# Kernel optimization log

Hardware: AMD Instinct MI355X
Metric: run time of the kernel (lower is better)

## Reference

```python
import jax, jax.numpy as jnp
import numpy as np

N_NODES = 50000
N_EDGES = 600000
D_IN = 128
DIM = 128
N_REL = 3
N_LAYERS = 2


def setup_inputs() -> dict:
    key = jax.random.key(0)
    ks = jax.random.split(key, 10)
    s = 1.0 / np.sqrt(DIM)
    x = jax.random.normal(ks[0], (N_NODES, D_IN), dtype=jnp.float32)
    edge_index = jax.random.randint(ks[1], (2, N_EDGES), 0, N_NODES)
    edge_type = jax.random.randint(ks[2], (N_EDGES,), 0, N_REL)
    edge_weight = jax.random.uniform(ks[3], (N_EDGES,), dtype=jnp.float32)
    # stacked per-layer parameters (layer dims are uniform since D_IN == DIM)
    w_rel = jax.random.normal(ks[4], (N_LAYERS, N_REL, DIM, DIM), dtype=jnp.float32) * s
    w_root = jax.random.normal(ks[5], (N_LAYERS, DIM, DIM), dtype=jnp.float32) * s
    b_conv = jnp.zeros((N_LAYERS, DIM), dtype=jnp.float32)
    w_skip = jax.random.normal(ks[6], (N_LAYERS, D_IN, DIM), dtype=jnp.float32) * s
    b_skip = jnp.zeros((N_LAYERS, DIM), dtype=jnp.float32)
    return {"x": x, "edge_index": edge_index, "edge_type": edge_type,
            "edge_weight": edge_weight, "w_rel": w_rel, "w_root": w_root,
            "b_conv": b_conv, "w_skip": w_skip, "b_skip": b_skip}


def reference(x, edge_index, edge_type, edge_weight, w_rel, w_root, b_conv, w_skip, b_skip):
    n = x.shape[0]
    src, dst = edge_index[0], edge_index[1]
    h = x
    for l in range(w_rel.shape[0]):  # small fixed layer loop (2)
        skip = x @ w_skip[l] + b_skip[l]                      # [N, dim]
        # per-relation transform of all nodes: [R, N, dim] (cheap GEMMs),
        # avoids materializing a per-edge [E, d, d] weight gather
        hr = jnp.einsum('nd,rde->rne', h, w_rel[l])
        msgs = hr[edge_type, src] * edge_weight[:, None]      # [E, dim] gather
        agg = jax.ops.segment_sum(msgs, dst, num_segments=n)  # scatter-add
        h = agg + h @ w_root[l] + b_conv[l] + skip            # conv + skip residual
    return h
```

## Files before the change

### kernel.cpp

```cpp
#include <hip/hip_runtime.h>


#define DIM 128
#define MAXDEG 40
#define K_CNTB 512
#define K_CONVB 2048

typedef short short8 __attribute__((ext_vector_type(8)));
typedef float f32x4 __attribute__((ext_vector_type(4)));

__device__ __forceinline__ unsigned short f2bf(float f) {
    unsigned u = __float_as_uint(f);
    unsigned r = (u + 0x7FFFu + ((u >> 16) & 1u)) >> 16;
    return (unsigned short)r;
}
__device__ __forceinline__ float bflo(unsigned p) { return __uint_as_float(p << 16); }
__device__ __forceinline__ float bfhi(unsigned p) { return __uint_as_float(p & 0xFFFF0000u); }

__device__ void prep_body(const float* __restrict__ w_rel, const float* __restrict__ w_root,
                          const float* __restrict__ w_skip, unsigned short* __restrict__ WTf,
                          int bid) {
    for (int i = bid * 256 + threadIdx.x; i < 2 * 5 * DIM * DIM; i += 256 * 256) {
        int j    = i & 7;
        int lane = (i >> 3) & 63;
        int ks   = (i >> 9) & 3;
        int n    = (i >> 11) & 7;
        int s    = (i >> 14) % 5;
        int l    = i / (5 * DIM * DIM);
        int col = n * 16 + (lane & 15);
        int k   = ks * 32 + (lane >> 4) * 8 + j;
        float v;
        if (s < 3)       v = w_rel[(((size_t)l * 3 + s) * DIM + k) * DIM + col];
        else if (s == 3) {
            v = w_root[((size_t)l * DIM + k) * DIM + col];
            if (l == 0) v += w_skip[((size_t)k) * DIM + col];
        } else           v = w_skip[((size_t)l * DIM + k) * DIM + col];
        WTf[i] = f2bf(v);
    }
}

__global__ __launch_bounds__(256) void prep_zero(
    const float* __restrict__ w_rel, const float* __restrict__ w_root,
    const float* __restrict__ w_skip, unsigned short* __restrict__ WTf,
    int4* __restrict__ zp, int n4) {
    int b = blockIdx.x;
    if (b < 256) prep_body(w_rel, w_root, w_skip, WTf, b);
    else {
        int i = (b - 256) * 256 + threadIdx.x;
        if (i < n4) zp[i] = make_int4(0, 0, 0, 0);
    }
}

__device__ void conv_body(const float* __restrict__ in, unsigned short* __restrict__ ob,
                          int n8, int bid) {
    for (int i = bid * 256 + threadIdx.x; i < n8; i += K_CONVB * 256) {
        const float4* ip = reinterpret_cast<const float4*>(in) + (size_t)i * 2;
        float4 v0 = ip[0], v1 = ip[1];
        uint4 o;
        o.x = (unsigned)f2bf(v0.x) | ((unsigned)f2bf(v0.y) << 16);
        o.y = (unsigned)f2bf(v0.z) | ((unsigned)f2bf(v0.w) << 16);
        o.z = (unsigned)f2bf(v1.x) | ((unsigned)f2bf(v1.y) << 16);
        o.w = (unsigned)f2bf(v1.z) | ((unsigned)f2bf(v1.w) << 16);
        reinterpret_cast<uint4*>(ob)[i] = o;
    }
}

__device__ void cntsct_body(const int* __restrict__ src, const int* __restrict__ dst,
                            const int* __restrict__ etype, const float* __restrict__ ew,
                            int* __restrict__ counts, unsigned* __restrict__ csrp,
                            int E, int bid) {
    for (int i = bid * 256 + threadIdx.x; i < E; i += K_CNTB * 256) {
        int d = dst[i];
        int r = atomicAdd(&counts[d], 1);
        unsigned wq = (unsigned)__float2uint_rn(ew[i] * 16383.0f);
        unsigned rec = (unsigned)src[i] | ((unsigned)etype[i] << 16) | (wq << 18);
        if (r < MAXDEG) csrp[(size_t)d * MAXDEG + r] = rec;
    }
}

template<bool HAS_SKIP, bool AF32>
__device__ void gemm_body(
    int bid,
    const void* __restrict__ Ap, const unsigned short* __restrict__ Xb,
    const unsigned short* __restrict__ WTf,
    const float* __restrict__ bconv, const float* __restrict__ bskip,
    unsigned short* __restrict__ hr, void* __restrict__ outp, int M) {
    constexpr int NF = HAS_SKIP ? 40 : 32;
    __shared__ unsigned short stile[4][32][136];
    int t = threadIdx.x, lane = t & 63, wid = t >> 6;
    int lrow = lane & 15, lhi = lane >> 4;
    int r0 = bid * 128 + wid * 32;

    short8 af[2][4];
    #pragma unroll
    for (int rg = 0; rg < 2; ++rg) {
        int r = r0 + rg * 16 + lrow;
        int rc = r < M ? r : 0;
        if (AF32) {
            const float* ap = (const float*)Ap + (size_t)rc * DIM + lhi * 8;
            #pragma unroll
            for (int ks = 0; ks < 4; ++ks) {
                float4 u = *reinterpret_cast<const float4*>(ap + ks * 32);
                float4 v = *reinterpret_cast<const float4*>(ap + ks * 32 + 4);
                short8 s;
                s[0] = (short)f2bf(u.x); s[1] = (short)f2bf(u.y);
                s[2] = (short)f2bf(u.z); s[3] = (short)f2bf(u.w);
                s[4] = (short)f2bf(v.x); s[5] = (short)f2bf(v.y);
                s[6] = (short)f2bf(v.z); s[7] = (short)f2bf(v.w);
                af[rg][ks] = s;
            }
        } else {
            const unsigned short* ap = (const unsigned short*)Ap + (size_t)rc * DIM + lhi * 8;
            #pragma unroll
            for (int ks = 0; ks < 4; ++ks)
                af[rg][ks] = *reinterpret_cast<const short8*>(ap + ks * 32);
        }
    }
    short8 xf[2][4];
    f32x4 acc34[2][8];

    auto flush = [&](unsigned short* gbase) {
        #pragma unroll
        for (int j = 0; j < 8; ++j) {
            int lr = j * 4 + lhi;
            int lc = lrow * 8;
            int gr = r0 + lr;
            if (gr < M)
                *reinterpret_cast<uint4*>(gbase + (size_t)gr * DIM + lc) =
                    *reinterpret_cast<const uint4*>(&stile[wid][lr][lc]);
        }
    };

    short8 b0[4], b1[4];
    auto loadB = [&](int fi, short8* bb) {
        const unsigned short* p = WTf + ((size_t)fi * 4 * 64 + lane) * 8;
        #pragma unroll
        for (int ks = 0; ks < 4; ++ks)
            bb[ks] = *reinterpret_cast<const short8*>(p + ks * 512);
    };
    loadB(0, b0);
    #pragma unroll
    for (int fi = 0; fi < NF; ++fi) {
        short8* bc = (fi & 1) ? b1 : b0;
        short8* bn = (fi & 1) ? b0 : b1;
        if (fi + 1 < NF) loadB(fi + 1, bn);
        const int slot = fi >> 3, n = fi & 7;
        const int col = n * 16 + lrow;
        if (HAS_SKIP && slot == 3 && n == 0) {
            #pragma unroll
            for (int rg = 0; rg < 2; ++rg) {
                int r = r0 + rg * 16 + lrow;
                const unsigned short* xp = Xb + (size_t)(r < M ? r : 0) * DIM + lhi * 8;
                #pragma unroll
                for (int ks = 0; ks < 4; ++ks)
                    xf[rg][ks] = *reinterpret_cast<const short8*>(xp + ks * 32);
            }
        }
        if (slot < 3) {
            f32x4 a0 = {0.f, 0.f, 0.f, 0.f}, a1 = {0.f, 0.f, 0.f, 0.f};
            #pragma unroll
            for (int ks = 0; ks < 4; ++ks) {
                a0 = __builtin_amdgcn_mfma_f32_16x16x32_bf16(af[0][ks], bc[ks], a0, 0, 0, 0);
                a1 = __builtin_amdgcn_mfma_f32_16x16x32_bf16(af[1][ks], bc[ks], a1, 0, 0, 0);
            }
            #pragma unroll
            for (int rg = 0; rg < 2; ++rg) {
                f32x4& aa = rg ? a1 : a0;
                #pragma unroll
                for (int i2 = 0; i2 < 4; ++i2)
                    stile[wid][rg * 16 + lhi * 4 + i2][col] = f2bf(aa[i2]);
            }
            if (n == 7) flush(hr + (size_t)slot * M * DIM);
        } else if (!HAS_SKIP) {
            f32x4 a0 = {0.f, 0.f, 0.f, 0.f}, a1 = {0.f, 0.f, 0.f, 0.f};
            #pragma unroll
            for (int ks = 0; ks < 4; ++ks) {
                a0 = __builtin_amdgcn_mfma_f32_16x16x32_bf16(af[0][ks], bc[ks], a0, 0, 0, 0);
                a1 = __builtin_amdgcn_mfma_f32_16x16x32_bf16(af[1][ks], bc[ks], a1, 0, 0, 0);
            }
            float bb = bconv[col] + bskip[col];
            #pragma unroll
            for (int rg = 0; rg < 2; ++rg) {
                f32x4& aa = rg ? a1 : a0;
                #pragma unroll
                for (int i2 = 0; i2 < 4; ++i2)
                    stile[wid][rg * 16 + lhi * 4 + i2][col] = f2bf(aa[i2] + bb);
            }
            if (n == 7) flush((unsigned short*)outp);
        } else if (slot == 3) {
            f32x4 z = {0.f, 0.f, 0.f, 0.f};
            acc34[0][n] = z; acc34[1][n] = z;
            #pragma unroll
            for (int ks = 0; ks < 4; ++ks) {
                acc34[0][n] = __builtin_amdgcn_mfma_f32_16x16x32_bf16(af[0][ks], bc[ks], acc34[0][n], 0, 0, 0);
                acc34[1][n] = __builtin_amdgcn_mfma_f32_16x16x32_bf16(af[1][ks], bc[ks], acc34[1][n], 0, 0, 0);
            }
        } else {
            #pragma unroll
            for (int ks = 0; ks < 4; ++ks) {
                acc34[0][n] = __builtin_amdgcn_mfma_f32_16x16x32_bf16(xf[0][ks], bc[ks], acc34[0][n], 0, 0, 0);
                acc34[1][n] = __builtin_amdgcn_mfma_f32_16x16x32_bf16(xf[1][ks], bc[ks], acc34[1][n], 0, 0, 0);
            }
            float bb = bconv[col] + bskip[col];
            float* op = (float*)outp;
            #pragma unroll
            for (int rg = 0; rg < 2; ++rg) {
                #pragma unroll
                for (int i2 = 0; i2 < 4; ++i2) {
                    int r = r0 + rg * 16 + lhi * 4 + i2;
                    if (r < M) op[(size_t)r * DIM + col] = acc34[rg][n][i2] + bb;
                }
            }
        }
    }
}

__global__ __launch_bounds__(256) void fat1_kernel(
    const float* __restrict__ x, const unsigned short* __restrict__ WTf,
    const float* __restrict__ bconv, const float* __restrict__ bskip,
    unsigned short* __restrict__ hr, unsigned short* __restrict__ h1, int M, int GB,
    const int* __restrict__ src, const int* __restrict__ dst,
    const int* __restrict__ etype, const float* __restrict__ ew,
    int* __restrict__ counts, unsigned* __restrict__ csrp, int E,
    unsigned short* __restrict__ xb, int n8) {
    int b = blockIdx.x;
    if (b < GB)
        gemm_body<false, true>(b, x, nullptr, WTf, bconv, bskip, hr, h1, M);
    else if (b < GB + K_CNTB)
        cntsct_body(src, dst, etype, ew, counts, csrp, E, b - GB);
    else
        conv_body(x, xb, n8, b - GB - K_CNTB);
}

__global__ __launch_bounds__(256) void gemm1_kernel(
    const unsigned short* __restrict__ Ab, const unsigned short* __restrict__ Xb,
    const unsigned short* __restrict__ WTf,
    const float* __restrict__ bconv, const float* __restrict__ bskip,
    unsigned short* __restrict__ hr, float* __restrict__ outp, int M) {
    gemm_body<true, false>(blockIdx.x, Ab, Xb, WTf, bconv, bskip, hr, outp, M);
}

template<bool BF16IO>
__global__ __launch_bounds__(256) void agg_kernel(
    const unsigned short* __restrict__ hr, const unsigned* __restrict__ csrp,
    const int* __restrict__ counts, float* __restrict__ outf,
    unsigned short* __restrict__ outb, int N) {
    int t = threadIdx.x;
    int lane = t & 63;
    int v = blockIdx.x * 4 + (t >> 6);
    if (v >= N) return;
    int g = lane >> 4;
    int l16 = lane & 15;
    int beg = v * MAXDEG;
    int cnt = counts[v]; if (cnt > MAXDEG) cnt = MAXDEG;
    int end = beg + cnt;

    float acc[8] = {0.f, 0.f, 0.f, 0.f, 0.f, 0.f, 0.f, 0.f};
    int iA = beg + g, iB = iA + 4;
    bool vA = iA < end, vB = iB < end;
    unsigned sA = vA ? csrp[iA] : 0u;
    unsigned sB = vB ? csrp[iB] : 0u;
    while (__any(vA)) {
        uint4 pA = make_uint4(0, 0, 0, 0), pB = make_uint4(0, 0, 0, 0);
        if (vA) {
            const unsigned short* row = hr + ((size_t)((sA >> 16) & 3) * N + (sA & 0xFFFF)) * DIM + l16 * 8;
            pA = *reinterpret_cast<const uint4*>(row);
        }
        if (vB) {
            const unsigned short* row = hr + ((size_t)((sB >> 16) & 3) * N + (sB & 0xFFFF)) * DIM + l16 * 8;
            pB = *reinterpret_cast<const uint4*>(row);
        }
        int nA = iA + 8, nB = iB + 8;
        bool nvA = nA < end, nvB = nB < end;
        unsigned nsA = nvA ? csrp[nA] : 0u;
        unsigned nsB = nvB ? csrp[nB] : 0u;
        if (vA) {
            float w = (float)(sA >> 18) * (1.0f / 16383.0f);
            acc[0] += w * bflo(pA.x); acc[1] += w * bfhi(pA.x);
            acc[2] += w * bflo(pA.y); acc[3] += w * bfhi(pA.y);
            acc[4] += w * bflo(pA.z); acc[5] += w * bfhi(pA.z);
            acc[6] += w * bflo(pA.w); acc[7] += w * bfhi(pA.w);
        }
        if (vB) {
            float w = (float)(sB >> 18) * (1.0f / 16383.0f);
            acc[0] += w * bflo(pB.x); acc[1] += w * bfhi(pB.x);
            acc[2] += w * bflo(pB.y); acc[3] += w * bfhi(pB.y);
            acc[4] += w * bflo(pB.z); acc[5] += w * bfhi(pB.z);
            acc[6] += w * bflo(pB.w); acc[7] += w * bfhi(pB.w);
        }
        iA = nA; iB = nB; sA = nsA; sB = nsB; vA = nvA; vB = nvB;
    }
    #pragma unroll
    for (int j = 0; j < 8; ++j) {
        acc[j] += __shfl_xor(acc[j], 16);
        acc[j] += __shfl_xor(acc[j], 32);
    }
    if (g == 0) {
        if (BF16IO) {
            unsigned short* op = outb + (size_t)v * DIM + l16 * 8;
            uint4 cur = *reinterpret_cast<const uint4*>(op);
            float r0 = bflo(cur.x) + acc[0], r1 = bfhi(cur.x) + acc[1];
            float r2 = bflo(cur.y) + acc[2], r3 = bfhi(cur.y) + acc[3];
            float r4 = bflo(cur.z) + acc[4], r5 = bfhi(cur.z) + acc[5];
            float r6 = bflo(cur.w) + acc[6], r7 = bfhi(cur.w) + acc[7];
            uint4 o;
            o.x = (unsigned)f2bf(r0) | ((unsigned)f2bf(r1) << 16);
            o.y = (unsigned)f2bf(r2) | ((unsigned)f2bf(r3) << 16);
            o.z = (unsigned)f2bf(r4) | ((unsigned)f2bf(r5) << 16);
            o.w = (unsigned)f2bf(r6) | ((unsigned)f2bf(r7) << 16);
            *reinterpret_cast<uint4*>(op) = o;
        } else {
            float* op = outf + (size_t)v * DIM + l16 * 8;
            float4 c0 = *reinterpret_cast<float4*>(op);
            float4 c1 = *reinterpret_cast<float4*>(op + 4);
            c0.x += acc[0]; c0.y += acc[1]; c0.z += acc[2]; c0.w += acc[3];
            c1.x += acc[4]; c1.y += acc[5]; c1.z += acc[6]; c1.w += acc[7];
            *reinterpret_cast<float4*>(op) = c0;
            *reinterpret_cast<float4*>(op + 4) = c1;
        }
    }
}

extern "C" void kernel_launch(void* const* d_in, const int* in_sizes, int n_in,
                              void* d_out, int out_size, void* d_ws, size_t ws_size,
                              hipStream_t stream) {
    const float* x       = (const float*)d_in[0];
    const int*   eidx    = (const int*)d_in[1];
    const int*   etype   = (const int*)d_in[2];
    const float* ew      = (const float*)d_in[3];
    const float* w_rel   = (const float*)d_in[4];
    const float* w_root  = (const float*)d_in[5];
    const float* b_conv  = (const float*)d_in[6];
    const float* w_skip  = (const float*)d_in[7];
    const float* b_skip  = (const float*)d_in[8];

    const int N = in_sizes[0] / DIM;
    const int E = in_sizes[3];
    const int* src = eidx;
    const int* dst = eidx + E;

    char* w = (char*)d_ws;
    unsigned short* WTf  = (unsigned short*)w;  w += (size_t)2 * 5 * DIM * DIM * 2;
    unsigned short* xb   = (unsigned short*)w;  w += (size_t)N * DIM * 2;
    unsigned short* hr   = (unsigned short*)w;  w += (size_t)3 * N * DIM * 2;
    unsigned short* h1   = (unsigned short*)w;  w += (size_t)N * DIM * 2;
    int* counts          = (int*)w;             w += (size_t)N * 4;
    unsigned* csrp       = (unsigned*)w;        w += (size_t)N * MAXDEG * 4;

    float* out = (float*)d_out;
    const int n8 = N * DIM / 8;
    const int zc = (N + 3) / 4;
    const int zblk = (zc + 255) / 256;

    prep_zero<<<256 + zblk, 256, 0, stream>>>(w_rel, w_root, w_skip, WTf,
                                              (int4*)counts, zc);
    int GB = (N + 127) / 128;
    fat1_kernel<<<GB + K_CNTB + K_CONVB, 256, 0, stream>>>(
        x, WTf, b_conv, b_skip, hr, h1, N, GB,
        src, dst, etype, ew, counts, csrp, E, xb, n8);
    int ablocks = (N + 3) / 4;
    agg_kernel<true><<<ablocks, 256, 0, stream>>>(hr, csrp, counts, nullptr, h1, N);
    gemm1_kernel<<<GB, 256, 0, stream>>>(h1, xb, WTf + (size_t)5 * DIM * DIM,
                                         b_conv + DIM, b_skip + DIM, hr, out, N);
    agg_kernel<false><<<ablocks, 256, 0, stream>>>(hr, csrp, counts, out, nullptr, N);
}
```

Measured before the change: 139.0 us.

## Overlap layer-1 skip GEMM with layer-0 aggregation in a fused launch

Pulls the layer-1 skip GEMM (x @ w_skip + biases) out of gemm1 and runs it in a new fat2 kernel alongside the layer-0 aggregation, since it depends only on x. gemm1 then computes only the relation and root transforms and adds the root result into the output in place. This shortens the critical-path GEMM and fills idle compute during the memory-bound aggregation. The cost is an extra read-modify-write of the fp32 output in gemm1.

```diff
diff --git a/kernel.cpp b/kernel.cpp
--- a/kernel.cpp
+++ b/kernel.cpp
@@ -78,14 +78,11 @@
     }
 }
 
-template<bool HAS_SKIP, bool AF32>
-__device__ void gemm_body(
-    int bid,
-    const void* __restrict__ Ap, const unsigned short* __restrict__ Xb,
+__device__ void gemm0_body(
+    int bid, const float* __restrict__ Ap,
     const unsigned short* __restrict__ WTf,
     const float* __restrict__ bconv, const float* __restrict__ bskip,
-    unsigned short* __restrict__ hr, void* __restrict__ outp, int M) {
-    constexpr int NF = HAS_SKIP ? 40 : 32;
+    unsigned short* __restrict__ hr, unsigned short* __restrict__ h1, int M) {
     __shared__ unsigned short stile[4][32][136];
     int t = threadIdx.x, lane = t & 63, wid = t >> 6;
     int lrow = lane & 15, lhi = lane >> 4;
@@ -96,41 +93,28 @@
     for (int rg = 0; rg < 2; ++rg) {
         int r = r0 + rg * 16 + lrow;
         int rc = r < M ? r : 0;
-        if (AF32) {
-            const float* ap = (const float*)Ap + (size_t)rc * DIM + lhi * 8;
-            #pragma unroll
-            for (int ks = 0; ks < 4; ++ks) {
-                float4 u = *reinterpret_cast<const float4*>(ap + ks * 32);
-                float4 v = *reinterpret_cast<const float4*>(ap + ks * 32 + 4);
-                short8 s;
-                s[0] = (short)f2bf(u.x); s[1] = (short)f2bf(u.y);
-                s[2] = (short)f2bf(u.z); s[3] = (short)f2bf(u.w);
-                s[4] = (short)f2bf(v.x); s[5] = (short)f2bf(v.y);
-                s[6] = (short)f2bf(v.z); s[7] = (short)f2bf(v.w);
-                af[rg][ks] = s;
-            }
-        } else {
-            const unsigned short* ap = (const unsigned short*)Ap + (size_t)rc * DIM + lhi * 8;
-            #pragma unroll
-            for (int ks = 0; ks < 4; ++ks)
-                af[rg][ks] = *reinterpret_cast<const short8*>(ap + ks * 32);
-        }
-    }
-    short8 xf[2][4];
-    f32x4 acc34[2][8];
-
+        const float* ap = Ap + (size_t)rc * DIM + lhi * 8;
+        #pragma unroll
+        for (int ks = 0; ks < 4; ++ks) {
+            float4 u = *reinterpret_cast<const float4*>(ap + ks * 32);
+            float4 v = *reinterpret_cast<const float4*>(ap + ks * 32 + 4);
+            short8 s;
+            s[0] = (short)f2bf(u.x); s[1] = (short)f2bf(u.y);
+            s[2] = (short)f2bf(u.z); s[3] = (short)f2bf(u.w);
+            s[4] = (short)f2bf(v.x); s[5] = (short)f2bf(v.y);
+            s[6] = (short)f2bf(v.z); s[7] = (short)f2bf(v.w);
+            af[rg][ks] = s;
+        }
+    }
     auto flush = [&](unsigned short* gbase) {
         #pragma unroll
         for (int j = 0; j < 8; ++j) {
-            int lr = j * 4 + lhi;
-            int lc = lrow * 8;
-            int gr = r0 + lr;
+            int lr = j * 4 + lhi, gr = r0 + lr;
             if (gr < M)
-                *reinterpret_cast<uint4*>(gbase + (size_t)gr * DIM + lc) =
-                    *reinterpret_cast<const uint4*>(&stile[wid][lr][lc]);
+                *reinterpret_cast<uint4*>(gbase + (size_t)gr * DIM + lrow * 8) =
+                    *reinterpret_cast<const uint4*>(&stile[wid][lr][lrow * 8]);
         }
     };
-
     short8 b0[4], b1[4];
     auto loadB = [&](int fi, short8* bb) {
         const unsigned short* p = WTf + ((size_t)fi * 4 * 64 + lane) * 8;
@@ -140,29 +124,19 @@
     };
     loadB(0, b0);
     #pragma unroll
-    for (int fi = 0; fi < NF; ++fi) {
+    for (int fi = 0; fi < 32; ++fi) {
         short8* bc = (fi & 1) ? b1 : b0;
         short8* bn = (fi & 1) ? b0 : b1;
-        if (fi + 1 < NF) loadB(fi + 1, bn);
+        if (fi + 1 < 32) loadB(fi + 1, bn);
         const int slot = fi >> 3, n = fi & 7;
         const int col = n * 16 + lrow;
-        if (HAS_SKIP && slot == 3 && n == 0) {
-            #pragma unroll
-            for (int rg = 0; rg < 2; ++rg) {
-                int r = r0 + rg * 16 + lrow;
-                const unsigned short* xp = Xb + (size_t)(r < M ? r : 0) * DIM + lhi * 8;
-                #pragma unroll
-                for (int ks = 0; ks < 4; ++ks)
-                    xf[rg][ks] = *reinterpret_cast<const short8*>(xp + ks * 32);
-            }
+        f32x4 a0 = {0.f, 0.f, 0.f, 0.f}, a1 = {0.f, 0.f, 0.f, 0.f};
+        #pragma unroll
+        for (int ks = 0; ks < 4; ++ks) {
+            a0 = __builtin_amdgcn_mfma_f32_16x16x32_bf16(af[0][ks], bc[ks], a0, 0, 0, 0);
+            a1 = __builtin_amdgcn_mfma_f32_16x16x32_bf16(af[1][ks], bc[ks], a1, 0, 0, 0);
         }
         if (slot < 3) {
-            f32x4 a0 = {0.f, 0.f, 0.f, 0.f}, a1 = {0.f, 0.f, 0.f, 0.f};
-            #pragma unroll
-            for (int ks = 0; ks < 4; ++ks) {
-                a0 = __builtin_amdgcn_mfma_f32_16x16x32_bf16(af[0][ks], bc[ks], a0, 0, 0, 0);
-                a1 = __builtin_amdgcn_mfma_f32_16x16x32_bf16(af[1][ks], bc[ks], a1, 0, 0, 0);
-            }
             #pragma unroll
             for (int rg = 0; rg < 2; ++rg) {
                 f32x4& aa = rg ? a1 : a0;
@@ -171,13 +145,7 @@
                     stile[wid][rg * 16 + lhi * 4 + i2][col] = f2bf(aa[i2]);
             }
             if (n == 7) flush(hr + (size_t)slot * M * DIM);
-        } else if (!HAS_SKIP) {
-            f32x4 a0 = {0.f, 0.f, 0.f, 0.f}, a1 = {0.f, 0.f, 0.f, 0.f};
-            #pragma unroll
-            for (int ks = 0; ks < 4; ++ks) {
-                a0 = __builtin_amdgcn_mfma_f32_16x16x32_bf16(af[0][ks], bc[ks], a0, 0, 0, 0);
-                a1 = __builtin_amdgcn_mfma_f32_16x16x32_bf16(af[1][ks], bc[ks], a1, 0, 0, 0);
-            }
+        } else {
             float bb = bconv[col] + bskip[col];
             #pragma unroll
             for (int rg = 0; rg < 2; ++rg) {
@@ -186,31 +154,7 @@
                 for (int i2 = 0; i2 < 4; ++i2)
                     stile[wid][rg * 16 + lhi * 4 + i2][col] = f2bf(aa[i2] + bb);
             }
-            if (n == 7) flush((unsigned short*)outp);
-        } else if (slot == 3) {
-            f32x4 z = {0.f, 0.f, 0.f, 0.f};
-            acc34[0][n] = z; acc34[1][n] = z;
-            #pragma unroll
-            for (int ks = 0; ks < 4; ++ks) {
-                acc34[0][n] = __builtin_amdgcn_mfma_f32_16x16x32_bf16(af[0][ks], bc[ks], acc34[0][n], 0, 0, 0);
-                acc34[1][n] = __builtin_amdgcn_mfma_f32_16x16x32_bf16(af[1][ks], bc[ks], acc34[1][n], 0, 0, 0);
-            }
-        } else {
-            #pragma unroll
-            for (int ks = 0; ks < 4; ++ks) {
-                acc34[0][n] = __builtin_amdgcn_mfma_f32_16x16x32_bf16(xf[0][ks], bc[ks], acc34[0][n], 0, 0, 0);
-                acc34[1][n] = __builtin_amdgcn_mfma_f32_16x16x32_bf16(xf[1][ks], bc[ks], acc34[1][n], 0, 0, 0);
-            }
-            float bb = bconv[col] + bskip[col];
-            float* op = (float*)outp;
-            #pragma unroll
-            for (int rg = 0; rg < 2; ++rg) {
-                #pragma unroll
-                for (int i2 = 0; i2 < 4; ++i2) {
-                    int r = r0 + rg * 16 + lhi * 4 + i2;
-                    if (r < M) op[(size_t)r * DIM + col] = acc34[rg][n][i2] + bb;
-                }
-            }
+            if (n == 7) flush(h1);
         }
     }
 }
@@ -225,29 +169,21 @@
     unsigned short* __restrict__ xb, int n8) {
     int b = blockIdx.x;
     if (b < GB)
-        gemm_body<false, true>(b, x, nullptr, WTf, bconv, bskip, hr, h1, M);
+        gemm0_body(b, x, WTf, bconv, bskip, hr, h1, M);
     else if (b < GB + K_CNTB)
         cntsct_body(src, dst, etype, ew, counts, csrp, E, b - GB);
     else
         conv_body(x, xb, n8, b - GB - K_CNTB);
 }
 
-__global__ __launch_bounds__(256) void gemm1_kernel(
-    const unsigned short* __restrict__ Ab, const unsigned short* __restrict__ Xb,
-    const unsigned short* __restrict__ WTf,
-    const float* __restrict__ bconv, const float* __restrict__ bskip,
-    unsigned short* __restrict__ hr, float* __restrict__ outp, int M) {
-    gemm_body<true, false>(blockIdx.x, Ab, Xb, WTf, bconv, bskip, hr, outp, M);
-}
-
 template<bool BF16IO>
-__global__ __launch_bounds__(256) void agg_kernel(
-    const unsigned short* __restrict__ hr, const unsigned* __restrict__ csrp,
+__device__ void agg_body(
+    int bid, const unsigned short* __restrict__ hr, const unsigned* __restrict__ csrp,
     const int* __restrict__ counts, float* __restrict__ outf,
     unsigned short* __restrict__ outb, int N) {
     int t = threadIdx.x;
     int lane = t & 63;
-    int v = blockIdx.x * 4 + (t >> 6);
+    int v = bid * 4 + (t >> 6);
     if (v >= N) return;
     int g = lane >> 4;
     int l16 = lane & 15;
@@ -321,6 +257,155 @@
     }
 }
 
+__device__ void skip1_body(int bid, const unsigned short* __restrict__ xb,
+                           const unsigned short* __restrict__ WTf1,
+                           const float* __restrict__ bconv, const float* __restrict__ bskip,
+                           float* __restrict__ out, int M) {
+    int t = threadIdx.x, lane = t & 63, wid = t >> 6;
+    int lrow = lane & 15, lhi = lane >> 4;
+    int r0 = bid * 128 + wid * 32;
+
+    short8 af[2][4];
+    #pragma unroll
+    for (int rg = 0; rg < 2; ++rg) {
+        int r = r0 + rg * 16 + lrow;
+        const unsigned short* ap = xb + (size_t)(r < M ? r : 0) * DIM + lhi * 8;
+        #pragma unroll
+        for (int ks = 0; ks < 4; ++ks)
+            af[rg][ks] = *reinterpret_cast<const short8*>(ap + ks * 32);
+    }
+    short8 b0[4], b1[4];
+    auto loadB = [&](int fi, short8* bb) {
+        const unsigned short* p = WTf1 + ((size_t)fi * 4 * 64 + lane) * 8;
+        #pragma unroll
+        for (int ks = 0; ks < 4; ++ks)
+            bb[ks] = *reinterpret_cast<const short8*>(p + ks * 512);
+    };
+    loadB(32, b0);
+    #pragma unroll
+    for (int n = 0; n < 8; ++n) {
+        short8* bc = (n & 1) ? b1 : b0;
+        short8* bn = (n & 1) ? b0 : b1;
+        if (n + 1 < 8) loadB(32 + n + 1, bn);
+        f32x4 a0 = {0.f, 0.f, 0.f, 0.f}, a1 = {0.f, 0.f, 0.f, 0.f};
+        #pragma unroll
+        for (int ks = 0; ks < 4; ++ks) {
+            a0 = __builtin_amdgcn_mfma_f32_16x16x32_bf16(af[0][ks], bc[ks], a0, 0, 0, 0);
+            a1 = __builtin_amdgcn_mfma_f32_16x16x32_bf16(af[1][ks], bc[ks], a1, 0, 0, 0);
+        }
+        int col = n * 16 + lrow;
+        float bb = bconv[col] + bskip[col];
+        #pragma unroll
+        for (int rg = 0; rg < 2; ++rg) {
+            f32x4& aa = rg ? a1 : a0;
+            #pragma unroll
+            for (int i2 = 0; i2 < 4; ++i2) {
+                int r = r0 + rg * 16 + lhi * 4 + i2;
+                if (r < M) out[(size_t)r * DIM + col] = aa[i2] + bb;
+            }
+        }
+    }
+}
+
+__global__ __launch_bounds__(256) void fat2_kernel(
+    const unsigned short* __restrict__ hr, const unsigned* __restrict__ csrp,
+    const int* __restrict__ counts, unsigned short* __restrict__ h1, int N, int AB,
+    const unsigned short* __restrict__ xb, const unsigned short* __restrict__ WTf1,
+    const float* __restrict__ bconv1, const float* __restrict__ bskip1,
+    float* __restrict__ out, int M) {
+    int b = blockIdx.x;
+    if (b < AB) agg_body<true>(b, hr, csrp, counts, nullptr, h1, N);
+    else        skip1_body(b - AB, xb, WTf1, bconv1, bskip1, out, M);
+}
+
+__global__ __launch_bounds__(256) void gemm1_kernel(
+    const unsigned short* __restrict__ Ab, const unsigned short* __restrict__ WTf1,
+    unsigned short* __restrict__ hr, float* __restrict__ outp, int M) {
+    __shared__ unsigned short stile[4][32][136];
+    int bid = blockIdx.x;
+    int t = threadIdx.x, lane = t & 63, wid = t >> 6;
+    int lrow = lane & 15, lhi = lane >> 4;
+    int r0 = bid * 128 + wid * 32;
+
+    short8 af[2][4];
+    #pragma unroll
+    for (int rg = 0; rg < 2; ++rg) {
+        int r = r0 + rg * 16 + lrow;
+        const unsigned short* ap = Ab + (size_t)(r < M ? r : 0) * DIM + lhi * 8;
+        #pragma unroll
+        for (int ks = 0; ks < 4; ++ks)
+            af[rg][ks] = *reinterpret_cast<const short8*>(ap + ks * 32);
+    }
+    f32x4 acc34[2][8];
+    auto flush = [&](unsigned short* gbase) {
+        #pragma unroll
+        for (int j = 0; j < 8; ++j) {
+            int lr = j * 4 + lhi, gr = r0 + lr;
+            if (gr < M)
+                *reinterpret_cast<uint4*>(gbase + (size_t)gr * DIM + lrow * 8) =
+                    *reinterpret_cast<const uint4*>(&stile[wid][lr][lrow * 8]);
+        }
+    };
+    short8 b0[4], b1[4];
+    auto loadB = [&](int fi, short8* bb) {
+        const unsigned short* p = WTf1 + ((size_t)fi * 4 * 64 + lane) * 8;
+        #pragma unroll
+        for (int ks = 0; ks < 4; ++ks)
+            bb[ks] = *reinterpret_cast<const short8*>(p + ks * 512);
+    };
+    loadB(0, b0);
+    #pragma unroll
+    for (int fi = 0; fi < 32; ++fi) {
+        short8* bc = (fi & 1) ? b1 : b0;
+        short8* bn = (fi & 1) ? b0 : b1;
+        if (fi + 1 < 32) loadB(fi + 1, bn);
+        const int slot = fi >> 3, n = fi & 7;
+        const int col = n * 16 + lrow;
+        if (slot < 3) {
+            f32x4 a0 = {0.f, 0.f, 0.f, 0.f}, a1 = {0.f, 0.f, 0.f, 0.f};
+            #pragma unroll
+            for (int ks = 0; ks < 4; ++ks) {
+                a0 = __builtin_amdgcn_mfma_f32_16x16x32_bf16(af[0][ks], bc[ks], a0, 0, 0, 0);
+                a1 = __builtin_amdgcn_mfma_f32_16x16x32_bf16(af[1][ks], bc[ks], a1, 0, 0, 0);
+            }
+            #pragma unroll
+            for (int rg = 0; rg < 2; ++rg) {
+                f32x4& aa = rg ? a1 : a0;
+                #pragma unroll
+                for (int i2 = 0; i2 < 4; ++i2)
+                    stile[wid][rg * 16 + lhi * 4 + i2][col] = f2bf(aa[i2]);
+            }
+            if (n == 7) flush(hr + (size_t)slot * M * DIM);
+        } else {
+            f32x4 z = {0.f, 0.f, 0.f, 0.f};
+            acc34[0][n] = z; acc34[1][n] = z;
+            #pragma unroll
+            for (int ks = 0; ks < 4; ++ks) {
+                acc34[0][n] = __builtin_amdgcn_mfma_f32_16x16x32_bf16(af[0][ks], bc[ks], acc34[0][n], 0, 0, 0);
+                acc34[1][n] = __builtin_amdgcn_mfma_f32_16x16x32_bf16(af[1][ks], bc[ks], acc34[1][n], 0, 0, 0);
+            }
+        }
+    }
+    #pragma unroll
+    for (int n = 0; n < 8; ++n) {
+        int col = n * 16 + lrow;
+        #pragma unroll
+        for (int rg = 0; rg < 2; ++rg) {
+            #pragma unroll
+            for (int i2 = 0; i2 < 4; ++i2) {
+                int r = r0 + rg * 16 + lhi * 4 + i2;
+                if (r < M) outp[(size_t)r * DIM + col] += acc34[rg][n][i2];
+            }
+        }
+    }
+}
+
+__global__ __launch_bounds__(256) void agg1_kernel(
+    const unsigned short* __restrict__ hr, const unsigned* __restrict__ csrp,
+    const int* __restrict__ counts, float* __restrict__ outf, int N) {
+    agg_body<false>(blockIdx.x, hr, csrp, counts, outf, nullptr, N);
+}
+
 extern "C" void kernel_launch(void* const* d_in, const int* in_sizes, int n_in,
                               void* d_out, int out_size, void* d_ws, size_t ws_size,
                               hipStream_t stream) {
@@ -348,6 +433,7 @@
     unsigned* csrp       = (unsigned*)w;        w += (size_t)N * MAXDEG * 4;
 
     float* out = (float*)d_out;
+    const unsigned short* WTf1 = WTf + (size_t)5 * DIM * DIM;
     const int n8 = N * DIM / 8;
     const int zc = (N + 3) / 4;
     const int zblk = (zc + 255) / 256;
@@ -358,9 +444,10 @@
     fat1_kernel<<<GB + K_CNTB + K_CONVB, 256, 0, stream>>>(
         x, WTf, b_conv, b_skip, hr, h1, N, GB,
         src, dst, etype, ew, counts, csrp, E, xb, n8);
-    int ablocks = (N + 3) / 4;
-    agg_kernel<true><<<ablocks, 256, 0, stream>>>(hr, csrp, counts, nullptr, h1, N);
-    gemm1_kernel<<<GB, 256, 0, stream>>>(h1, xb, WTf + (size_t)5 * DIM * DIM,
-                                         b_conv + DIM, b_skip + DIM, hr, out, N);
-    agg_kernel<false><<<ablocks, 256, 0, stream>>>(hr, csrp, counts, out, nullptr, N);
-}
+    int AB = (N + 3) / 4;
+    fat2_kernel<<<AB + GB, 256, 0, stream>>>(
+        hr, csrp, counts, h1, N, AB,
+        xb, WTf1, b_conv + DIM, b_skip + DIM, out, N);
+    gemm1_kernel<<<GB, 256, 0, stream>>>(h1, WTf1, hr, out, N);
+    agg1_kernel<<<AB, 256, 0, stream>>>(hr, csrp, counts, out, N);
+}
```

Result: slower. 173.1 us (+24.5%).
